# Kernel optimization log

Measured on AMD Instinct MI355X. Metric: run time of the kernel, lower is better.

The kernel has to match this reference:

```python
import jax, jax.numpy as jnp
import numpy as np

FP4_E2M1_VALUES = [0.0, 0.0625, 8.0, 1.0, 2.0, 3.0, 4.0, 6.0,
                   -0.0, -0.0625, -8.0, -1.0, -2.0, -3.0, -4.0, -6.0]

M, N, K = 4096, 4096, 4096


def setup_inputs() -> dict:
    key = jax.random.key(0)
    k1, k2 = jax.random.split(key)
    x = jax.random.normal(k1, (M, K), dtype=jnp.float16)
    # packed uint8 bytes stored as int32 (values in [0,256)); each byte holds
    # two fp4 indices: high nibble = even k, low nibble = odd k
    packed_weight = jax.random.randint(k2, (N, K // 2), 0, 256, dtype=jnp.int32)
    lut = jnp.array(FP4_E2M1_VALUES, dtype=jnp.float16)
    return {"x": x, "packed_weight": packed_weight, "lut": lut}


def reference(x, packed_weight, lut):
    # Dequantize: unpack nibbles along K, LUT lookup -> W [N, K] fp16
    n, kh = packed_weight.shape
    high = (packed_weight >> 4) & 15   # even k positions
    low = packed_weight & 15           # odd k positions
    idx = jnp.stack([high, low], axis=-1).reshape(n, 2 * kh)  # [N, K]
    w = lut[idx]                       # [N, K] fp16
    # GEMM with fp32 accumulation (Triton kernel accumulates in fp32), cast to fp16
    y = jnp.einsum('mk,nk->mn', x, w, preferred_element_type=jnp.float32)
    return y.astype(jnp.float16)
```

## Files before the change

kernel.cpp:

```cpp
#include <hip/hip_runtime.h>
#include <hip/hip_fp16.h>
#include <stdint.h>

#define M_DIM 4096
#define N_DIM 4096
#define K_DIM 4096
#define BM 128
#define BN 128
#define BK 32
#define KW (K_DIM / 2)

typedef _Float16 half8 __attribute__((ext_vector_type(8)));
typedef float f32x4 __attribute__((ext_vector_type(4)));

__device__ __forceinline__ uint32_t pk2(float a, float b) {
  auto h = __builtin_amdgcn_cvt_pkrtz(a, b);
  return __builtin_bit_cast(uint32_t, h);
}

__global__ __launch_bounds__(256) void cvt_x_kernel(const float4* __restrict__ xin,
                                                    uint2* __restrict__ xout) {
  const int i = blockIdx.x * 256 + threadIdx.x;
  const float4 v = xin[i];
  xout[i] = make_uint2(pk2(v.x, v.y), pk2(v.z, v.w));
}

template <bool PRECONV>
__global__ __launch_bounds__(256, 2) void fp4gemm_kernel(
    const void* __restrict__ xv,
    const int* __restrict__ pw,
    const float* __restrict__ lutf,
    float* __restrict__ out)
{
  __shared__ uint16_t ldsA[BM * BK];
  __shared__ uint16_t ldsB[BN * BK];
  __shared__ uint32_t lutp[256];

  const int tid  = threadIdx.x;
  const int lane = tid & 63;
  const int wave = tid >> 6;
  const int wm   = wave >> 1;
  const int wn   = wave & 1;
  const int m0 = blockIdx.y * BM;
  const int n0 = blockIdx.x * BN;

  {
    const int hi = (tid >> 4) & 15, lo = tid & 15;
    lutp[tid] = pk2(lutf[hi], lutf[lo]);
  }

  f32x4 acc[4][4];
#pragma unroll
  for (int i = 0; i < 4; ++i)
#pragma unroll
    for (int j = 0; j < 4; ++j) acc[i][j] = (f32x4){0.f, 0.f, 0.f, 0.f};

  const int rowB  = tid >> 1;
  const int halfB = tid & 1;

  for (int kt = 0; kt < K_DIM / BK; ++kt) {
    __syncthreads();

    if constexpr (PRECONV) {
      const uint8_t* xh = (const uint8_t*)xv;
#pragma unroll
      for (int s = 0; s < 2; ++s) {
        const int idx = tid + s * 256;
        const int row = idx >> 2;
        const int c16 = idx & 3;
        const uint8_t* gp = xh + ((size_t)(m0 + row) * K_DIM + kt * BK) * 2 + c16 * 16;
        uint8_t* lp = (uint8_t*)ldsA + (size_t)idx * 16;
        __builtin_amdgcn_global_load_lds(
            (const __attribute__((address_space(1))) uint32_t*)gp,
            (__attribute__((address_space(3))) uint32_t*)lp, 16, 0, 0);
      }
    } else {
      const float* xf = (const float*)xv;
#pragma unroll
      for (int s = 0; s < 4; ++s) {
        const int c   = tid + s * 256;
        const int row = c >> 3;
        const int c4  = c & 7;
        const float4 v = *(const float4*)(xf + (size_t)(m0 + row) * K_DIM + kt * BK + c4 * 4);
        *(uint2*)((uint8_t*)ldsA + row * 64 + c4 * 8) =
            make_uint2(pk2(v.x, v.y), pk2(v.z, v.w));
      }
    }

    {
      const int* gp = pw + (size_t)(n0 + rowB) * KW + kt * (BK / 2) + halfB * 8;
      const int4 wA = ((const int4*)gp)[0];
      const int4 wB = ((const int4*)gp)[1];
      const uint32_t p0 = lutp[wA.x & 255], p1 = lutp[wA.y & 255];
      const uint32_t p2 = lutp[wA.z & 255], p3 = lutp[wA.w & 255];
      const uint32_t p4 = lutp[wB.x & 255], p5 = lutp[wB.y & 255];
      const uint32_t p6 = lutp[wB.z & 255], p7 = lutp[wB.w & 255];
      uint32_t* lb = (uint32_t*)((uint8_t*)ldsB + rowB * 64 + halfB * 32);
      ((uint4*)lb)[0] = make_uint4(p0, p1, p2, p3);
      ((uint4*)lb)[1] = make_uint4(p4, p5, p6, p7);
    }

    __syncthreads();

    half8 af[4], bfr[4];
#pragma unroll
    for (int i = 0; i < 4; ++i) {
      const uint16_t* pa = ldsA + (wm * 64 + i * 16 + (lane & 15)) * BK + (lane >> 4) * 8;
      af[i] = *(const half8*)pa;
    }
#pragma unroll
    for (int j = 0; j < 4; ++j) {
      const uint16_t* pb = ldsB + (wn * 64 + j * 16 + (lane & 15)) * BK + (lane >> 4) * 8;
      bfr[j] = *(const half8*)pb;
    }
#pragma unroll
    for (int i = 0; i < 4; ++i)
#pragma unroll
      for (int j = 0; j < 4; ++j)
        acc[i][j] = __builtin_amdgcn_mfma_f32_16x16x32_f16(af[i], bfr[j], acc[i][j], 0, 0, 0);
  }

  const int mb = m0 + wm * 64 + (lane >> 4) * 4;
  const int nb = n0 + wn * 64 + (lane & 15);
#pragma unroll
  for (int i = 0; i < 4; ++i)
#pragma unroll
    for (int j = 0; j < 4; ++j)
#pragma unroll
      for (int r = 0; r < 4; ++r)
        out[(size_t)(mb + i * 16 + r) * N_DIM + (nb + j * 16)] = acc[i][j][r];
}

extern "C" void kernel_launch(void* const* d_in, const int* in_sizes, int n_in,
                              void* d_out, int out_size, void* d_ws, size_t ws_size,
                              hipStream_t stream) {
  const void* px = nullptr; const void* ppw = nullptr; const void* plut = nullptr;
  for (int i = 0; i < n_in; ++i) {
    const long s = in_sizes[i];
    if (s == (long)M_DIM * K_DIM) px = d_in[i];
    else if (s == (long)N_DIM * KW) ppw = d_in[i];
    else if (s == 16) plut = d_in[i];
  }
  if (!px || !ppw || !plut) { px = d_in[0]; ppw = d_in[1]; plut = d_in[2]; }

  dim3 grid(N_DIM / BN, M_DIM / BM);
  const size_t xh_bytes = (size_t)M_DIM * K_DIM * 2;

  if (ws_size >= xh_bytes) {
    cvt_x_kernel<<<(M_DIM * K_DIM / 4) / 256, 256, 0, stream>>>(
        (const float4*)px, (uint2*)d_ws);
    fp4gemm_kernel<true><<<grid, dim3(256), 0, stream>>>(
        d_ws, (const int*)ppw, (const float*)plut, (float*)d_out);
  } else {
    fp4gemm_kernel<false><<<grid, dim3(256), 0, stream>>>(
        px, (const int*)ppw, (const float*)plut, (float*)d_out);
  }
}
```

Before: 313.7 us.

## Fuse x conversion into GEMM and replace LDS LUT with register byte-permute dequant

Removes the separate fp32-to-fp16 conversion kernel for x. The GEMM now loads fp32 x directly, converts it in registers and writes fp16 into LDS, which saves a kernel launch and a workspace round trip. The LDS pair-lookup table is replaced by register-resident packed LUT bytes, decoded with v_perm plus sign-bit insertion. This relies on the LUT having symmetric signs and the low fp16 byte being zero. The A loads are now synchronous register loads instead of global_load_lds, and fp32 x traffic per tile doubles.

```diff
diff --git a/kernel.cpp b/kernel.cpp
--- a/kernel.cpp
+++ b/kernel.cpp
@@ -18,23 +18,28 @@
   return __builtin_bit_cast(uint32_t, h);
 }
 
-__global__ __launch_bounds__(256) void cvt_x_kernel(const float4* __restrict__ xin,
-                                                    uint2* __restrict__ xout) {
-  const int i = blockIdx.x * 256 + threadIdx.x;
-  const float4 v = xin[i];
-  xout[i] = make_uint2(pk2(v.x, v.y), pk2(v.z, v.w));
+__device__ __forceinline__ uint32_t dq(uint32_t b, uint32_t ph, uint32_t pl) {
+#if __has_builtin(__builtin_amdgcn_perm)
+  const uint32_t sel = ((b & 0x70u) << 4) | ((b & 0x07u) << 24);
+  uint32_t v = __builtin_amdgcn_perm(ph, pl, sel);
+#else
+  const uint64_t pool = ((uint64_t)ph << 32) | pl;
+  const uint32_t mh = (uint32_t)(pool >> (((b >> 4) & 7u) * 8)) & 0xFFu;
+  const uint32_t ml = (uint32_t)(pool >> ((b & 7u) * 8)) & 0xFFu;
+  uint32_t v = (mh << 8) | (ml << 24);
+#endif
+  const uint32_t sg = ((b & 0x88u) * 0x10000100u) & 0x80008000u;
+  return v | sg;
 }
 
-template <bool PRECONV>
 __global__ __launch_bounds__(256, 2) void fp4gemm_kernel(
-    const void* __restrict__ xv,
+    const float* __restrict__ xf,
     const int* __restrict__ pw,
     const float* __restrict__ lutf,
     float* __restrict__ out)
 {
   __shared__ uint16_t ldsA[BM * BK];
   __shared__ uint16_t ldsB[BN * BK];
-  __shared__ uint32_t lutp[256];
 
   const int tid  = threadIdx.x;
   const int lane = tid & 63;
@@ -44,10 +49,19 @@
   const int m0 = blockIdx.y * BM;
   const int n0 = blockIdx.x * BN;
 
-  {
-    const int hi = (tid >> 4) & 15, lo = tid & 15;
-    lutp[tid] = pk2(lutf[hi], lutf[lo]);
-  }
+  const uint32_t h01 = pk2(lutf[0], lutf[1]);
+  const uint32_t h23 = pk2(lutf[2], lutf[3]);
+  const uint32_t h45 = pk2(lutf[4], lutf[5]);
+  const uint32_t h67 = pk2(lutf[6], lutf[7]);
+#if __has_builtin(__builtin_amdgcn_perm)
+  const uint32_t pl = __builtin_amdgcn_perm(h23, h01, 0x07050301u);
+  const uint32_t ph = __builtin_amdgcn_perm(h67, h45, 0x07050301u);
+#else
+  const uint32_t pl = ((h01 >> 8) & 0xFFu) | ((h01 >> 24) << 8) |
+                      (((h23 >> 8) & 0xFFu) << 16) | ((h23 >> 24) << 24);
+  const uint32_t ph = ((h45 >> 8) & 0xFFu) | ((h45 >> 24) << 8) |
+                      (((h67 >> 8) & 0xFFu) << 16) | ((h67 >> 24) << 24);
+#endif
 
   f32x4 acc[4][4];
 #pragma unroll
@@ -61,43 +75,28 @@
   for (int kt = 0; kt < K_DIM / BK; ++kt) {
     __syncthreads();
 
-    if constexpr (PRECONV) {
-      const uint8_t* xh = (const uint8_t*)xv;
 #pragma unroll
-      for (int s = 0; s < 2; ++s) {
-        const int idx = tid + s * 256;
-        const int row = idx >> 2;
-        const int c16 = idx & 3;
-        const uint8_t* gp = xh + ((size_t)(m0 + row) * K_DIM + kt * BK) * 2 + c16 * 16;
-        uint8_t* lp = (uint8_t*)ldsA + (size_t)idx * 16;
-        __builtin_amdgcn_global_load_lds(
-            (const __attribute__((address_space(1))) uint32_t*)gp,
-            (__attribute__((address_space(3))) uint32_t*)lp, 16, 0, 0);
-      }
-    } else {
-      const float* xf = (const float*)xv;
-#pragma unroll
-      for (int s = 0; s < 4; ++s) {
-        const int c   = tid + s * 256;
-        const int row = c >> 3;
-        const int c4  = c & 7;
-        const float4 v = *(const float4*)(xf + (size_t)(m0 + row) * K_DIM + kt * BK + c4 * 4);
-        *(uint2*)((uint8_t*)ldsA + row * 64 + c4 * 8) =
-            make_uint2(pk2(v.x, v.y), pk2(v.z, v.w));
-      }
+    for (int s = 0; s < 2; ++s) {
+      const int c   = tid + s * 256;
+      const int row = c >> 2;
+      const int c16 = c & 3;
+      const float* gp = xf + (size_t)(m0 + row) * K_DIM + kt * BK + c16 * 8;
+      const float4 v0 = *(const float4*)gp;
+      const float4 v1 = *(const float4*)(gp + 4);
+      *(uint4*)((uint8_t*)ldsA + row * 64 + c16 * 16) =
+          make_uint4(pk2(v0.x, v0.y), pk2(v0.z, v0.w),
+                     pk2(v1.x, v1.y), pk2(v1.z, v1.w));
     }
 
     {
       const int* gp = pw + (size_t)(n0 + rowB) * KW + kt * (BK / 2) + halfB * 8;
       const int4 wA = ((const int4*)gp)[0];
       const int4 wB = ((const int4*)gp)[1];
-      const uint32_t p0 = lutp[wA.x & 255], p1 = lutp[wA.y & 255];
-      const uint32_t p2 = lutp[wA.z & 255], p3 = lutp[wA.w & 255];
-      const uint32_t p4 = lutp[wB.x & 255], p5 = lutp[wB.y & 255];
-      const uint32_t p6 = lutp[wB.z & 255], p7 = lutp[wB.w & 255];
       uint32_t* lb = (uint32_t*)((uint8_t*)ldsB + rowB * 64 + halfB * 32);
-      ((uint4*)lb)[0] = make_uint4(p0, p1, p2, p3);
-      ((uint4*)lb)[1] = make_uint4(p4, p5, p6, p7);
+      ((uint4*)lb)[0] = make_uint4(dq(wA.x, ph, pl), dq(wA.y, ph, pl),
+                                   dq(wA.z, ph, pl), dq(wA.w, ph, pl));
+      ((uint4*)lb)[1] = make_uint4(dq(wB.x, ph, pl), dq(wB.y, ph, pl),
+                                   dq(wB.z, ph, pl), dq(wB.w, ph, pl));
     }
 
     __syncthreads();
@@ -144,15 +143,6 @@
   if (!px || !ppw || !plut) { px = d_in[0]; ppw = d_in[1]; plut = d_in[2]; }
 
   dim3 grid(N_DIM / BN, M_DIM / BM);
-  const size_t xh_bytes = (size_t)M_DIM * K_DIM * 2;
-
-  if (ws_size >= xh_bytes) {
-    cvt_x_kernel<<<(M_DIM * K_DIM / 4) / 256, 256, 0, stream>>>(
-        (const float4*)px, (uint2*)d_ws);
-    fp4gemm_kernel<true><<<grid, dim3(256), 0, stream>>>(
-        d_ws, (const int*)ppw, (const float*)plut, (float*)d_out);
-  } else {
-    fp4gemm_kernel<false><<<grid, dim3(256), 0, stream>>>(
-        px, (const int*)ppw, (const float*)plut, (float*)d_out);
-  }
+  fp4gemm_kernel<<<grid, dim3(256), 0, stream>>>(
+      (const float*)px, (const int*)ppw, (const float*)plut, (float*)d_out);
 }
```

New measurement: 398.8 us. +27.1%, slower.
